# Kernel tuning notes

Measured on AMD Instinct MI355X. Metric: run time of the kernel, lower is better.

The kernel has to match this reference:

```python
import jax, jax.numpy as jnp
import numpy as np

N, L, S, D, K, H, G = 512, 1024, 3, 128, 4, 32, 64


def setup_inputs() -> dict:
    key = jax.random.key(0)
    ks = jax.random.split(key, 12)
    f = lambda i, shape, s=1.0: jax.random.normal(ks[i], shape, dtype=jnp.float32) * s
    return dict(
        scores=f(0, (N, 1, L, S)),
        veh_repr=f(1, (N, 1, D)),
        cust_repr=f(2, (N, L, D)),
        edge_emb=f(3, (N, 1, L, D)),
        expert_w1=f(4, (K, S, H), 0.3),
        expert_b1=jnp.zeros((K, H), jnp.float32),
        expert_w2=f(5, (K, H, 1), 0.3),
        expert_b2=jnp.zeros((K, 1), jnp.float32),
        sit_w1=f(6, (2 * D, G), 0.05),
        sit_b1=jnp.zeros((G,), jnp.float32),
        sit_w2=f(7, (G, K), 0.1),
        sit_b2=jnp.zeros((K,), jnp.float32),
        cand_w=f(8, (S, K), 0.3),
        cand_b=jnp.zeros((K,), jnp.float32),
        edge_w=f(9, (D, K), 0.05),
        gate_balance=jnp.zeros((), jnp.float32),
    )


def reference(scores, veh_repr, cust_repr, edge_emb,
              expert_w1, expert_b1, expert_w2, expert_b2,
              sit_w1, sit_b1, sit_w2, sit_b2,
              cand_w, cand_b, edge_w, gate_balance):
    # Inference mode: no gate noise, no dropout (identity at eval).
    # Situation gating: vehicle repr + graph context -> (N,1,K) logits
    graph_ctx = cust_repr.mean(axis=1, keepdims=True)              # (N,1,D)
    sit_in = jnp.concatenate([veh_repr, graph_ctx], axis=-1)       # (N,1,2D)
    hg = jax.nn.gelu(sit_in @ sit_w1 + sit_b1, approximate=False)  # (N,1,G)
    sit_logits = hg @ sit_w2 + sit_b2                              # (N,1,K)

    # Candidate-level gating from raw scores + edge embeddings
    cand_logits = scores @ cand_w + cand_b + edge_emb @ edge_w     # (N,1,L,K)

    alpha = jax.nn.sigmoid(gate_balance)
    gate_logits = alpha * sit_logits[:, :, None, :] + (1.0 - alpha) * cand_logits
    gate_w = jax.nn.softmax(gate_logits, axis=-1)                  # (N,1,L,K)

    # Per-expert tiny MLP over the S score channels
    h = jax.nn.gelu(jnp.einsum('nqls,ksh->nqlkh', scores, expert_w1) + expert_b1,
                    approximate=False)                             # (N,1,L,K,H)
    expert_out = jnp.einsum('nqlkh,kho->nqlko', h, expert_w2)[..., 0] + expert_b2[:, 0]

    fused = (gate_w * expert_out).sum(axis=-1)                     # (N,1,L)
    return fused
```

## Files before the change

### kernel.cpp

```cpp
#include <hip/hip_runtime.h>

#define NN 512
#define LL 1024
#define SS 3
#define DD 128
#define KK 4
#define HH 32
#define GG 64

__device__ __forceinline__ float fast_gelu(float x) {
    const float c0 = 0.7978845608028654f;
    const float c1 = 0.7978845608028654f * 0.044715f;
    float u = x * x;
    float y = x * fmaf(c1, u, c0);
    float e = __expf(2.0f * y);
    float r = __builtin_amdgcn_rcpf(e + 1.0f);
    float t = fmaf(-2.0f, r, 1.0f);
    return 0.5f * x * (1.0f + t);
}

__global__ __launch_bounds__(512, 4) void k_all(
    const float* __restrict__ scores, const float* __restrict__ veh,
    const float* __restrict__ cust, const float* __restrict__ edge,
    const float* __restrict__ ew1, const float* __restrict__ eb1,
    const float* __restrict__ ew2, const float* __restrict__ eb2,
    const float* __restrict__ sw1, const float* __restrict__ sb1,
    const float* __restrict__ sw2, const float* __restrict__ sb2,
    const float* __restrict__ cand_w, const float* __restrict__ cand_b,
    const float* __restrict__ edge_w, const float* __restrict__ gbp,
    float* __restrict__ out)
{
    __shared__ float4 red[512];
    __shared__ float sin_[2 * DD];
    __shared__ float hg[GG];
    __shared__ float slds[KK];

    const int n = blockIdx.x;
    const int t = threadIdx.x;
    const int lane = t & 63;
    const int r = lane & 31;

    const int ko = r & 3;
    const int jg = r >> 2;
    const bool kb0 = (r & 1) != 0;
    const bool kb1 = (r & 2) != 0;
    const float4* ew4 = (const float4*)edge_w;
    const float4 wqa = ew4[4 * r + 0];
    const float4 wqb = ew4[4 * r + 1];
    const float4 wqc = ew4[4 * r + 2];
    const float4 wqd = ew4[4 * r + 3];
    const float cw0 = cand_w[0 * KK + ko];
    const float cw1 = cand_w[1 * KK + ko];
    const float cw2 = cand_w[2 * KK + ko];
    const float cb  = cand_b[ko];
    const float4* w1f = (const float4*)ew1;
    const float4 w1a = w1f[(ko * SS + 0) * (HH / 4) + jg];
    const float4 w1b = w1f[(ko * SS + 1) * (HH / 4) + jg];
    const float4 w1c = w1f[(ko * SS + 2) * (HH / 4) + jg];
    const float4 b1v = ((const float4*)eb1)[ko * (HH / 4) + jg];
    const float4 w2v = ((const float4*)ew2)[ko * (HH / 4) + jg];
    const float b2o = eb2[ko];
    const float gbv = gbp[0];
    const float alpha = 1.0f / (1.0f + __expf(-gbv));
    const float onema = 1.0f - alpha;

    const int c = t & 31;
    const int rs = t >> 5;
    const float4* cp = (const float4*)(cust + (size_t)n * LL * DD);
    float4 a0 = make_float4(0.f, 0.f, 0.f, 0.f), a1 = a0, a2 = a0, a3 = a0;
    #pragma unroll 4
    for (int i = 0; i < 16; ++i) {
        float4 v0 = cp[(rs + 16 * i      ) * 32 + c];
        float4 v1 = cp[(rs + 16 * i + 256) * 32 + c];
        float4 v2 = cp[(rs + 16 * i + 512) * 32 + c];
        float4 v3 = cp[(rs + 16 * i + 768) * 32 + c];
        a0.x += v0.x; a0.y += v0.y; a0.z += v0.z; a0.w += v0.w;
        a1.x += v1.x; a1.y += v1.y; a1.z += v1.z; a1.w += v1.w;
        a2.x += v2.x; a2.y += v2.y; a2.z += v2.z; a2.w += v2.w;
        a3.x += v3.x; a3.y += v3.y; a3.z += v3.z; a3.w += v3.w;
    }
    a0.x += a1.x + a2.x + a3.x;
    a0.y += a1.y + a2.y + a3.y;
    a0.z += a1.z + a2.z + a3.z;
    a0.w += a1.w + a2.w + a3.w;
    red[t] = a0;
    __syncthreads();

    if (t < 32) {
        float4 s = red[t];
        #pragma unroll
        for (int i = 1; i < 16; i++) {
            float4 v = red[i * 32 + t];
            s.x += v.x; s.y += v.y; s.z += v.z; s.w += v.w;
        }
        const float inv = 1.0f / (float)LL;
        sin_[DD + 4 * t + 0] = s.x * inv;
        sin_[DD + 4 * t + 1] = s.y * inv;
        sin_[DD + 4 * t + 2] = s.z * inv;
        sin_[DD + 4 * t + 3] = s.w * inv;
        float4 vv = ((const float4*)(veh + (size_t)n * DD))[t];
        sin_[4 * t + 0] = vv.x; sin_[4 * t + 1] = vv.y;
        sin_[4 * t + 2] = vv.z; sin_[4 * t + 3] = vv.w;
    }
    __syncthreads();

    if (t < GG) {
        float a = sb1[t];
        #pragma unroll 8
        for (int i = 0; i < 2 * DD; i++)
            a = fmaf(sin_[i], sw1[i * GG + t], a);
        hg[t] = fast_gelu(a);
    }
    __syncthreads();
    if (t < KK) {
        float a = sb2[t];
        #pragma unroll
        for (int g = 0; g < GG; g++)
            a = fmaf(hg[g], sw2[g * KK + t], a);
        slds[t] = a;
    }
    __syncthreads();

    const float sl0 = slds[0], sl1 = slds[1], sl2 = slds[2], sl3 = slds[3];
    float sa_ = kb0 ? sl1 : sl0;
    float sb_ = kb0 ? sl3 : sl2;
    float so  = kb1 ? sb_ : sa_;
    const float sbase = fmaf(alpha, so, onema * cb);

    const int w = t >> 6;
    const int half = lane >> 5;
    const float* sc_base = scores + (size_t)n * LL * SS;
    const float* ed_base = edge + (size_t)n * LL * DD;
    float* out_base = out + (size_t)n * LL;

    for (int i = 0; i < 64; ++i) {
        const int el = w * 2 + half + i * 16;
        const float4 ev = *(const float4*)(ed_base + (size_t)el * DD + r * 4);
        float p0 = ev.x * wqa.x; p0 = fmaf(ev.y, wqb.x, p0); p0 = fmaf(ev.z, wqc.x, p0); p0 = fmaf(ev.w, wqd.x, p0);
        float p1 = ev.x * wqa.y; p1 = fmaf(ev.y, wqb.y, p1); p1 = fmaf(ev.z, wqc.y, p1); p1 = fmaf(ev.w, wqd.y, p1);
        float p2 = ev.x * wqa.z; p2 = fmaf(ev.y, wqb.z, p2); p2 = fmaf(ev.z, wqc.z, p2); p2 = fmaf(ev.w, wqd.z, p2);
        float p3 = ev.x * wqa.w; p3 = fmaf(ev.y, wqb.w, p3); p3 = fmaf(ev.z, wqc.w, p3); p3 = fmaf(ev.w, wqd.w, p3);
        p0 += __shfl_xor(p0, 1); p1 += __shfl_xor(p1, 1); p2 += __shfl_xor(p2, 1); p3 += __shfl_xor(p3, 1);
        p0 += __shfl_xor(p0, 2); p1 += __shfl_xor(p1, 2); p2 += __shfl_xor(p2, 2); p3 += __shfl_xor(p3, 2);
        float qa = kb0 ? p1 : p0;
        float qb = kb0 ? p3 : p2;
        float q  = kb1 ? qb : qa;
        q += __shfl_xor(q, 4); q += __shfl_xor(q, 8); q += __shfl_xor(q, 16);

        const float s0 = sc_base[el * 3 + 0];
        const float s1 = sc_base[el * 3 + 1];
        const float s2 = sc_base[el * 3 + 2];

        const float sdot = fmaf(s0, cw0, fmaf(s1, cw1, s2 * cw2));
        const float gl = fmaf(onema, sdot + q, sbase);

        float m = gl;
        m = fmaxf(m, __shfl_xor(m, 1));
        m = fmaxf(m, __shfl_xor(m, 2));
        float ex = __expf(gl - m);
        float se = ex;
        se += __shfl_xor(se, 1);
        se += __shfl_xor(se, 2);
        float gw = ex * __builtin_amdgcn_rcpf(se);

        float acc;
        {
            float z, h;
            z = fmaf(s0, w1a.x, fmaf(s1, w1b.x, fmaf(s2, w1c.x, b1v.x))); h = fast_gelu(z); acc = h * w2v.x;
            z = fmaf(s0, w1a.y, fmaf(s1, w1b.y, fmaf(s2, w1c.y, b1v.y))); h = fast_gelu(z); acc = fmaf(h, w2v.y, acc);
            z = fmaf(s0, w1a.z, fmaf(s1, w1b.z, fmaf(s2, w1c.z, b1v.z))); h = fast_gelu(z); acc = fmaf(h, w2v.z, acc);
            z = fmaf(s0, w1a.w, fmaf(s1, w1b.w, fmaf(s2, w1c.w, b1v.w))); h = fast_gelu(z); acc = fmaf(h, w2v.w, acc);
        }
        acc += __shfl_xor(acc, 4); acc += __shfl_xor(acc, 8); acc += __shfl_xor(acc, 16);

        float tk = gw * (acc + b2o);
        tk += __shfl_xor(tk, 1);
        tk += __shfl_xor(tk, 2);
        if (r == 0) out_base[el] = tk;
    }
}

extern "C" void kernel_launch(void* const* d_in, const int* in_sizes, int n_in,
                              void* d_out, int out_size, void* d_ws, size_t ws_size,
                              hipStream_t stream)
{
    const float* scores = (const float*)d_in[0];
    const float* veh    = (const float*)d_in[1];
    const float* cust   = (const float*)d_in[2];
    const float* edge   = (const float*)d_in[3];
    const float* ew1    = (const float*)d_in[4];
    const float* eb1    = (const float*)d_in[5];
    const float* ew2    = (const float*)d_in[6];
    const float* eb2    = (const float*)d_in[7];
    const float* sw1    = (const float*)d_in[8];
    const float* sb1    = (const float*)d_in[9];
    const float* sw2    = (const float*)d_in[10];
    const float* sb2    = (const float*)d_in[11];
    const float* cw     = (const float*)d_in[12];
    const float* cb     = (const float*)d_in[13];
    const float* egw    = (const float*)d_in[14];
    const float* gb     = (const float*)d_in[15];
    float* out = (float*)d_out;

    hipLaunchKernelGGL(k_all, dim3(NN), dim3(512), 0, stream,
                       scores, veh, cust, edge, ew1, eb1, ew2, eb2,
                       sw1, sb1, sw2, sb2, cw, cb, egw, gb, out);
}
```

Before: 577.7 us.

## Unroll candidate loop by four and use ds_swizzle butterfly reductions

The main candidate loop now handles four elements per iteration, issuing their edge-embedding and score loads together for memory-level parallelism. Lane reductions switch from __shfl_xor to ds_swizzle, and the per-k projection reduction becomes a select-and-exchange transpose. The softmax max-subtraction is dropped, and the expert output and gate-weighted sum are folded into a single 32-lane reduction, with the bias scaled by 1/8. Together these cut cross-lane traffic and latency stalls, at the cost of more registers and possible exp overflow for large logits.

Result: faster. 559.4 us (-3.2%).

```diff
diff --git a/kernel.cpp b/kernel.cpp
--- a/kernel.cpp
+++ b/kernel.cpp
@@ -7,6 +7,16 @@
 #define KK 4
 #define HH 32
 #define GG 64
+
+#define SWZ1  0x041F
+#define SWZ2  0x081F
+#define SWZ4  0x101F
+#define SWZ8  0x201F
+#define SWZ16 0x401F
+template <int IMM>
+__device__ __forceinline__ float swz(float x) {
+    return __int_as_float(__builtin_amdgcn_ds_swizzle(__float_as_int(x), IMM));
+}
 
 __device__ __forceinline__ float fast_gelu(float x) {
     const float c0 = 0.7978845608028654f;
@@ -44,6 +54,7 @@
     const int jg = r >> 2;
     const bool kb0 = (r & 1) != 0;
     const bool kb1 = (r & 2) != 0;
+
     const float4* ew4 = (const float4*)edge_w;
     const float4 wqa = ew4[4 * r + 0];
     const float4 wqb = ew4[4 * r + 1];
@@ -59,7 +70,7 @@
     const float4 w1c = w1f[(ko * SS + 2) * (HH / 4) + jg];
     const float4 b1v = ((const float4*)eb1)[ko * (HH / 4) + jg];
     const float4 w2v = ((const float4*)ew2)[ko * (HH / 4) + jg];
-    const float b2o = eb2[ko];
+    const float b2o8 = 0.125f * eb2[ko];
     const float gbv = gbp[0];
     const float alpha = 1.0f / (1.0f + __expf(-gbv));
     const float onema = 1.0f - alpha;
@@ -127,56 +138,98 @@
     float so  = kb1 ? sb_ : sa_;
     const float sbase = fmaf(alpha, so, onema * cb);
 
-    const int w = t >> 6;
-    const int half = lane >> 5;
+    const int base_el = t >> 5;
     const float* sc_base = scores + (size_t)n * LL * SS;
     const float* ed_base = edge + (size_t)n * LL * DD;
     float* out_base = out + (size_t)n * LL;
 
-    for (int i = 0; i < 64; ++i) {
-        const int el = w * 2 + half + i * 16;
-        const float4 ev = *(const float4*)(ed_base + (size_t)el * DD + r * 4);
-        float p0 = ev.x * wqa.x; p0 = fmaf(ev.y, wqb.x, p0); p0 = fmaf(ev.z, wqc.x, p0); p0 = fmaf(ev.w, wqd.x, p0);
-        float p1 = ev.x * wqa.y; p1 = fmaf(ev.y, wqb.y, p1); p1 = fmaf(ev.z, wqc.y, p1); p1 = fmaf(ev.w, wqd.y, p1);
-        float p2 = ev.x * wqa.z; p2 = fmaf(ev.y, wqb.z, p2); p2 = fmaf(ev.z, wqc.z, p2); p2 = fmaf(ev.w, wqd.z, p2);
-        float p3 = ev.x * wqa.w; p3 = fmaf(ev.y, wqb.w, p3); p3 = fmaf(ev.z, wqc.w, p3); p3 = fmaf(ev.w, wqd.w, p3);
-        p0 += __shfl_xor(p0, 1); p1 += __shfl_xor(p1, 1); p2 += __shfl_xor(p2, 1); p3 += __shfl_xor(p3, 1);
-        p0 += __shfl_xor(p0, 2); p1 += __shfl_xor(p1, 2); p2 += __shfl_xor(p2, 2); p3 += __shfl_xor(p3, 2);
-        float qa = kb0 ? p1 : p0;
-        float qb = kb0 ? p3 : p2;
-        float q  = kb1 ? qb : qa;
-        q += __shfl_xor(q, 4); q += __shfl_xor(q, 8); q += __shfl_xor(q, 16);
-
-        const float s0 = sc_base[el * 3 + 0];
-        const float s1 = sc_base[el * 3 + 1];
-        const float s2 = sc_base[el * 3 + 2];
-
-        const float sdot = fmaf(s0, cw0, fmaf(s1, cw1, s2 * cw2));
-        const float gl = fmaf(onema, sdot + q, sbase);
-
-        float m = gl;
-        m = fmaxf(m, __shfl_xor(m, 1));
-        m = fmaxf(m, __shfl_xor(m, 2));
-        float ex = __expf(gl - m);
-        float se = ex;
-        se += __shfl_xor(se, 1);
-        se += __shfl_xor(se, 2);
-        float gw = ex * __builtin_amdgcn_rcpf(se);
-
-        float acc;
-        {
-            float z, h;
-            z = fmaf(s0, w1a.x, fmaf(s1, w1b.x, fmaf(s2, w1c.x, b1v.x))); h = fast_gelu(z); acc = h * w2v.x;
-            z = fmaf(s0, w1a.y, fmaf(s1, w1b.y, fmaf(s2, w1c.y, b1v.y))); h = fast_gelu(z); acc = fmaf(h, w2v.y, acc);
-            z = fmaf(s0, w1a.z, fmaf(s1, w1b.z, fmaf(s2, w1c.z, b1v.z))); h = fast_gelu(z); acc = fmaf(h, w2v.z, acc);
-            z = fmaf(s0, w1a.w, fmaf(s1, w1b.w, fmaf(s2, w1c.w, b1v.w))); h = fast_gelu(z); acc = fmaf(h, w2v.w, acc);
-        }
-        acc += __shfl_xor(acc, 4); acc += __shfl_xor(acc, 8); acc += __shfl_xor(acc, 16);
-
-        float tk = gw * (acc + b2o);
-        tk += __shfl_xor(tk, 1);
-        tk += __shfl_xor(tk, 2);
-        if (r == 0) out_base[el] = tk;
+    for (int i = 0; i < 16; ++i) {
+        const int e0 = base_el + i * 64;
+        float4 ev[4];
+        float s0[4], s1[4], s2[4];
+        #pragma unroll
+        for (int u = 0; u < 4; ++u)
+            ev[u] = *(const float4*)(ed_base + (size_t)(e0 + u * 16) * DD + r * 4);
+        #pragma unroll
+        for (int u = 0; u < 4; ++u) {
+            const int el = e0 + u * 16;
+            s0[u] = sc_base[el * 3 + 0];
+            s1[u] = sc_base[el * 3 + 1];
+            s2[u] = sc_base[el * 3 + 2];
+        }
+
+        float p0[4], p1[4], p2[4], p3[4];
+        #pragma unroll
+        for (int u = 0; u < 4; ++u) {
+            p0[u] = fmaf(ev[u].x, wqa.x, fmaf(ev[u].y, wqb.x, fmaf(ev[u].z, wqc.x, ev[u].w * wqd.x)));
+            p1[u] = fmaf(ev[u].x, wqa.y, fmaf(ev[u].y, wqb.y, fmaf(ev[u].z, wqc.y, ev[u].w * wqd.y)));
+            p2[u] = fmaf(ev[u].x, wqa.z, fmaf(ev[u].y, wqb.z, fmaf(ev[u].z, wqc.z, ev[u].w * wqd.z)));
+            p3[u] = fmaf(ev[u].x, wqa.w, fmaf(ev[u].y, wqb.w, fmaf(ev[u].z, wqc.w, ev[u].w * wqd.w)));
+        }
+        float P0[4], P2[4];
+        #pragma unroll
+        for (int u = 0; u < 4; ++u) {
+            float g0 = kb0 ? p0[u] : p1[u];
+            float g2 = kb0 ? p2[u] : p3[u];
+            float k0 = kb0 ? p1[u] : p0[u];
+            float k2 = kb0 ? p3[u] : p2[u];
+            P0[u] = k0 + swz<SWZ1>(g0);
+            P2[u] = k2 + swz<SWZ1>(g2);
+        }
+        float q[4];
+        #pragma unroll
+        for (int u = 0; u < 4; ++u) {
+            float gv = kb1 ? P0[u] : P2[u];
+            float kv = kb1 ? P2[u] : P0[u];
+            q[u] = kv + swz<SWZ2>(gv);
+        }
+        #pragma unroll
+        for (int u = 0; u < 4; ++u) q[u] += swz<SWZ4>(q[u]);
+        #pragma unroll
+        for (int u = 0; u < 4; ++u) q[u] += swz<SWZ8>(q[u]);
+        #pragma unroll
+        for (int u = 0; u < 4; ++u) q[u] += swz<SWZ16>(q[u]);
+
+        float ex[4];
+        #pragma unroll
+        for (int u = 0; u < 4; ++u) {
+            float sdot = fmaf(s0[u], cw0, fmaf(s1[u], cw1, s2[u] * cw2));
+            float gl = fmaf(onema, sdot + q[u], sbase);
+            ex[u] = __expf(gl);
+        }
+        float se[4];
+        #pragma unroll
+        for (int u = 0; u < 4; ++u) se[u] = ex[u] + swz<SWZ1>(ex[u]);
+        #pragma unroll
+        for (int u = 0; u < 4; ++u) se[u] += swz<SWZ2>(se[u]);
+
+        float tk[4];
+        #pragma unroll
+        for (int u = 0; u < 4; ++u) {
+            float gw = ex[u] * __builtin_amdgcn_rcpf(se[u]);
+            float z, h, acc;
+            z = fmaf(s0[u], w1a.x, fmaf(s1[u], w1b.x, fmaf(s2[u], w1c.x, b1v.x))); h = fast_gelu(z); acc = h * w2v.x;
+            z = fmaf(s0[u], w1a.y, fmaf(s1[u], w1b.y, fmaf(s2[u], w1c.y, b1v.y))); h = fast_gelu(z); acc = fmaf(h, w2v.y, acc);
+            z = fmaf(s0[u], w1a.z, fmaf(s1[u], w1b.z, fmaf(s2[u], w1c.z, b1v.z))); h = fast_gelu(z); acc = fmaf(h, w2v.z, acc);
+            z = fmaf(s0[u], w1a.w, fmaf(s1[u], w1b.w, fmaf(s2[u], w1c.w, b1v.w))); h = fast_gelu(z); acc = fmaf(h, w2v.w, acc);
+            tk[u] = gw * (acc + b2o8);
+        }
+        #pragma unroll
+        for (int u = 0; u < 4; ++u) tk[u] += swz<SWZ1>(tk[u]);
+        #pragma unroll
+        for (int u = 0; u < 4; ++u) tk[u] += swz<SWZ2>(tk[u]);
+        #pragma unroll
+        for (int u = 0; u < 4; ++u) tk[u] += swz<SWZ4>(tk[u]);
+        #pragma unroll
+        for (int u = 0; u < 4; ++u) tk[u] += swz<SWZ8>(tk[u]);
+        #pragma unroll
+        for (int u = 0; u < 4; ++u) tk[u] += swz<SWZ16>(tk[u]);
+
+        if (r == 0) {
+            #pragma unroll
+            for (int u = 0; u < 4; ++u)
+                out_base[e0 + u * 16] = tk[u];
+        }
     }
 }
 
```
